# Kernel tuning notes

Measured on AMD Instinct MI355X. Metric: run time of the kernel, lower is better.

## Reference

```python
import jax, jax.numpy as jnp
import numpy as np

N = 100000       # nodes
E = 1600000      # edges
V = 50000        # vocab
H = 256          # embedding dim (hsize)
A = 64           # per-head out dim (asize)
NH = 3           # num_heads
G = 64           # graphs in batch


def setup_inputs() -> dict:
    key = jax.random.key(0)
    ks = jax.random.split(key, 12)
    h0 = jax.random.randint(ks[0], (N,), 0, V)
    src = jax.random.randint(ks[1], (E,), 0, N)
    dst = jax.random.randint(ks[2], (E,), 0, N)
    graph_ids = jnp.sort(jax.random.randint(ks[3], (N,), 0, G))
    s = 0.05
    emb = jax.random.normal(ks[4], (V, H), jnp.float32) * s
    W_fc = jax.random.normal(ks[5], (H, NH * A), jnp.float32) * s   # GATConv fc
    attn_l = jax.random.normal(ks[6], (NH, A), jnp.float32) * s
    attn_r = jax.random.normal(ks[7], (NH, A), jnp.float32) * s
    bias_gat = jax.random.normal(ks[8], (NH, A), jnp.float32) * s
    W1 = jax.random.normal(ks[9], (A, 128), jnp.float32) * s
    b1 = jnp.zeros((128,), jnp.float32)
    W2 = jax.random.normal(ks[10], (128, 16), jnp.float32) * s
    b2 = jnp.zeros((16,), jnp.float32)
    return dict(h0=h0, src=src, dst=dst, graph_ids=graph_ids, emb=emb,
                W_fc=W_fc, attn_l=attn_l, attn_r=attn_r, bias_gat=bias_gat,
                W1=W1, b1=b1, W2=W2, b2=b2)


def reference(h0, src, dst, graph_ids, emb, W_fc, attn_l, attn_r, bias_gat,
              W1, b1, W2, b2):
    # embedding lookup
    h1 = emb[h0]                                            # [N, H]
    # GATConv: linear projection per head
    feat = (h1 @ W_fc).reshape(N, NH, A)                    # [N, NH, A]
    el = jnp.einsum('nha,ha->nh', feat, attn_l)             # [N, NH]
    er = jnp.einsum('nha,ha->nh', feat, attn_r)             # [N, NH]
    e = jax.nn.leaky_relu(el[src] + er[dst], 0.2)           # [E, NH]
    # segment softmax over incoming edges of each dst node
    m = jax.ops.segment_max(e, dst, num_segments=N)         # [N, NH]
    e_exp = jnp.exp(e - m[dst])                             # [E, NH]
    denom = jax.ops.segment_sum(e_exp, dst, num_segments=N) # [N, NH]
    alpha = e_exp / denom[dst]                              # [E, NH]
    # scatter-aggregate messages
    msg = alpha[:, :, None] * feat[src]                     # [E, NH, A]
    rst = jax.ops.segment_sum(msg, dst, num_segments=N)     # [N, NH, A]
    rst = rst + bias_gat[None]                              # GATConv bias
    # relu + mean over heads
    h2 = jnp.mean(jax.nn.relu(rst), axis=1)                 # [N, A]
    # MLP predictor: ReLU then Identity
    h3 = jax.nn.relu(h2 @ W1 + b1) @ W2 + b2                # [N, 16]
    # dgl.mean_nodes: per-graph mean readout
    sums = jax.ops.segment_sum(h3, graph_ids, num_segments=G)            # [G, 16]
    counts = jax.ops.segment_sum(jnp.ones((N,), h3.dtype), graph_ids, num_segments=G)
    return sums / jnp.maximum(counts, 1.0)[:, None]         # [G, 16]
```

## Files before the change

kernel.cpp:

```cpp
#include <hip/hip_runtime.h>
#include <hip/hip_bf16.h>

#define NNODES 100000
#define NEDGES 1600000
#define VOCAB 50000
#define HDIM 256
#define ADIM 64
#define NHEADS 3
#define FDIM 192
#define NGRAPH 64
#define NPART 64

#define CONV_ELEMS (HDIM * FDIM + 128 * 64 + 16 * 128)
#define CONV_BLOCKS ((CONV_ELEMS + 255) / 256)
#define ELVR_BLOCKS ((VOCAB + 3) / 4)
#define HIST_BLOCKS ((NEDGES + 255) / 256)
#define PROJ_BLOCKS ((VOCAB + 63) / 64)

typedef __attribute__((ext_vector_type(8))) short bf16x8;
typedef __attribute__((ext_vector_type(4))) float f32x4;

__device__ __forceinline__ float bf2f(unsigned short u) {
  return __uint_as_float((unsigned int)u << 16);
}
__device__ __forceinline__ unsigned short f2bf(float f) {
  unsigned int u = __float_as_uint(f);
  u += 0x7FFFu + ((u >> 16) & 1u);
  return (unsigned short)(u >> 16);
}

__global__ __launch_bounds__(256) void prep_kernel(
    const float* __restrict__ Wfc, const float* __restrict__ al,
    const float* __restrict__ ar, float* __restrict__ wl, float* __restrict__ wr)
{
  int t = blockIdx.x * 256 + threadIdx.x;
  if (t >= 3 * 256) return;
  int h = t >> 8, k = t & 255;
  const float* a_l = &al[h * 64];
  const float* a_r = &ar[h * 64];
  const float* row = &Wfc[(size_t)k * FDIM + h * 64];
  float sl = 0.f, sr = 0.f;
#pragma unroll 16
  for (int c = 0; c < 64; ++c) {
    float w = row[c];
    sl += w * a_l[c];
    sr += w * a_r[c];
  }
  wl[h * 256 + k] = sl;
  wr[h * 256 + k] = sr;
}

__global__ __launch_bounds__(256) void conv_elvr_hist_kernel(
    const float* __restrict__ Wfc, const float* __restrict__ W1,
    const float* __restrict__ W2, unsigned short* __restrict__ Wt,
    unsigned short* __restrict__ W1t, unsigned short* __restrict__ W2t,
    const float* __restrict__ emb, const float* __restrict__ wl,
    const float* __restrict__ wr, float4* __restrict__ elv4,
    float4* __restrict__ erv4,
    const int* __restrict__ dst, int* __restrict__ cnt,
    unsigned short* __restrict__ rank16)
{
  if (blockIdx.x < CONV_BLOCKS) {
    int i = blockIdx.x * 256 + threadIdx.x;
    if (i < HDIM * FDIM) {
      int c = i / HDIM, k = i % HDIM;
      Wt[i] = f2bf(Wfc[(size_t)k * FDIM + c]);
    } else if (i < HDIM * FDIM + 128 * 64) {
      int j = i - HDIM * FDIM;
      int c = j / 64, k = j % 64;
      W1t[j] = f2bf(W1[(size_t)k * 128 + c]);
    } else if (i < CONV_ELEMS) {
      int j = i - HDIM * FDIM - 128 * 64;
      int c = j / 128, k = j % 128;
      W2t[j] = f2bf(W2[(size_t)k * 16 + c]);
    }
    return;
  }
  if (blockIdx.x < CONV_BLOCKS + ELVR_BLOCKS) {
    int v = (blockIdx.x - CONV_BLOCKS) * 4 + (threadIdx.x >> 6);
    int lane = threadIdx.x & 63;
    if (v >= VOCAB) return;
    const float* er_ = &emb[(size_t)v * HDIM];
    float e0 = er_[lane], e1 = er_[64 + lane], e2 = er_[128 + lane], e3 = er_[192 + lane];
    float sl[3], sr[3];
#pragma unroll
    for (int h = 0; h < 3; ++h) {
      const float* wlh = &wl[h * 256];
      const float* wrh = &wr[h * 256];
      sl[h] = e0 * wlh[lane] + e1 * wlh[64 + lane] + e2 * wlh[128 + lane] + e3 * wlh[192 + lane];
      sr[h] = e0 * wrh[lane] + e1 * wrh[64 + lane] + e2 * wrh[128 + lane] + e3 * wrh[192 + lane];
    }
#pragma unroll
    for (int s = 32; s > 0; s >>= 1) {
#pragma unroll
      for (int h = 0; h < 3; ++h) {
        sl[h] += __shfl_xor(sl[h], s, 64);
        sr[h] += __shfl_xor(sr[h], s, 64);
      }
    }
    if (lane == 0) {
      elv4[v] = make_float4(sl[0], sl[1], sl[2], 0.f);
      erv4[v] = make_float4(sr[0], sr[1], sr[2], 0.f);
    }
    return;
  }
  int e = (blockIdx.x - CONV_BLOCKS - ELVR_BLOCKS) * 256 + threadIdx.x;
  if (e < NEDGES) rank16[e] = (unsigned short)atomicAdd(&cnt[dst[e]], 1);
}

__global__ __launch_bounds__(256) void scan_sum_kernel(
    const int* __restrict__ cnt, int* __restrict__ bsum, int n)
{
  __shared__ int red[256];
  int t = threadIdx.x;
  int base = blockIdx.x * 1024 + t * 4;
  int s = 0;
#pragma unroll
  for (int j = 0; j < 4; ++j) if (base + j < n) s += cnt[base + j];
  red[t] = s;
  __syncthreads();
  for (int o = 128; o > 0; o >>= 1) {
    if (t < o) red[t] += red[t + o];
    __syncthreads();
  }
  if (t == 0) bsum[blockIdx.x] = red[0];
}

__global__ void scan_bsum_kernel(int* bsum, int nb)
{
  if (threadIdx.x == 0 && blockIdx.x == 0) {
    int acc = 0;
    for (int i = 0; i < nb; ++i) { int v = bsum[i]; bsum[i] = acc; acc += v; }
  }
}

__global__ __launch_bounds__(256) void scan_write_kernel(
    const int* __restrict__ cnt, const int* __restrict__ bsum,
    int* __restrict__ offs, int n, int total)
{
  __shared__ int sd[256];
  int t = threadIdx.x;
  int base = blockIdx.x * 1024 + t * 4;
  int c[4];
  int ts = 0;
#pragma unroll
  for (int j = 0; j < 4; ++j) { c[j] = (base + j < n) ? cnt[base + j] : 0; ts += c[j]; }
  sd[t] = ts;
  __syncthreads();
  for (int o = 1; o < 256; o <<= 1) {
    int v = (t >= o) ? sd[t - o] : 0;
    __syncthreads();
    sd[t] += v;
    __syncthreads();
  }
  int run = sd[t] - ts + bsum[blockIdx.x];
#pragma unroll
  for (int j = 0; j < 4; ++j) {
    if (base + j < n) offs[base + j] = run;
    run += c[j];
  }
  if (blockIdx.x == 0 && t == 0) offs[n] = total;
}

__global__ __launch_bounds__(256) void proj_scatter_kernel(
    const float* __restrict__ emb,
    const unsigned short* __restrict__ Wt,
    unsigned short* __restrict__ proj_bf,
    const int* __restrict__ src, const int* __restrict__ dst,
    const int* __restrict__ h0, const unsigned short* __restrict__ rank16,
    const int* __restrict__ offs,
    const float4* __restrict__ elv4, const float4* __restrict__ erv4,
    uint2* __restrict__ wrec)
{
  if (blockIdx.x >= PROJ_BLOCKS) {
    int e = (blockIdx.x - PROJ_BLOCKS) * 256 + threadIdx.x;
    if (e < NEDGES) {
      int s = src[e], d = dst[e];
      unsigned vs = (unsigned)h0[s];
      float4 el = elv4[vs];
      float4 er = erv4[(unsigned)h0[d]];
      float e0 = el.x + er.x, e1 = el.y + er.y, e2 = el.z + er.z;
      e0 = e0 > 0.f ? e0 : 0.2f * e0;
      e1 = e1 > 0.f ? e1 : 0.2f * e1;
      e2 = e2 > 0.f ? e2 : 0.2f * e2;
      unsigned short u0 = f2bf(__expf(e0));
      unsigned short u1 = f2bf(__expf(e1));
      unsigned short u2 = f2bf(__expf(e2));
      int p = offs[d] + (int)rank16[e];
      wrec[p] = make_uint2(vs | ((unsigned)u0 << 16),
                           (unsigned)u1 | ((unsigned)u2 << 16));
    }
    return;
  }
  const int wave = threadIdx.x >> 6;
  const int lane = threadIdx.x & 63;
  const int row0 = blockIdx.x * 64 + wave * 16;
  const int cb = lane & 15;
  const int q  = lane >> 4;
  int arow = row0 + cb;
  if (arow >= VOCAB) arow = VOCAB - 1;
  const int kgrp = q * 8;

  f32x4 acc[12];
#pragma unroll
  for (int c = 0; c < 12; ++c) acc[c] = (f32x4){0.f, 0.f, 0.f, 0.f};

  const float* arow_p = &emb[(size_t)arow * HDIM + kgrp];
  const unsigned short* bcol_p = &Wt[(size_t)cb * HDIM + kgrp];

#pragma unroll
  for (int ks = 0; ks < 8; ++ks) {
    float4 f0 = *reinterpret_cast<const float4*>(arow_p + ks * 32);
    float4 f1 = *reinterpret_cast<const float4*>(arow_p + ks * 32 + 4);
    bf16x8 a;
    a[0] = (short)f2bf(f0.x); a[1] = (short)f2bf(f0.y);
    a[2] = (short)f2bf(f0.z); a[3] = (short)f2bf(f0.w);
    a[4] = (short)f2bf(f1.x); a[5] = (short)f2bf(f1.y);
    a[6] = (short)f2bf(f1.z); a[7] = (short)f2bf(f1.w);
#pragma unroll
    for (int c = 0; c < 12; ++c) {
      bf16x8 b = *reinterpret_cast<const bf16x8*>(bcol_p + (size_t)c * 16 * HDIM + ks * 32);
      acc[c] = __builtin_amdgcn_mfma_f32_16x16x32_bf16(a, b, acc[c], 0, 0, 0);
    }
  }

  const int rb = row0 + 4 * q;
#pragma unroll
  for (int i = 0; i < 4; ++i) {
    int r = rb + i;
    if (r < VOCAB) {
#pragma unroll
      for (int c = 0; c < 12; ++c)
        proj_bf[(size_t)r * FDIM + c * 16 + cb] = f2bf(acc[c][i]);
    }
  }
}

__global__ __launch_bounds__(256) void aggregate_kernel(
    const uint2* __restrict__ wrec, const int* __restrict__ offs,
    const unsigned short* __restrict__ proj_bf, const float* __restrict__ bias_gat,
    unsigned short* __restrict__ h2bf, int N)
{
  int lane = threadIdx.x & 63;
  int n = blockIdx.x * 4 + (threadIdx.x >> 6);
  if (n >= N) return;
  int lo = offs[n], hi = offs[n + 1];
  float a0 = 0.f, a1 = 0.f, a2 = 0.f, d0 = 0.f, d1 = 0.f, d2 = 0.f;

  int i = lo;
  for (; i + 4 <= hi; i += 4) {
    uint2 r[4];
#pragma unroll
    for (int j = 0; j < 4; ++j) r[j] = wrec[i + j];
    const unsigned short* ps[4];
#pragma unroll
    for (int j = 0; j < 4; ++j)
      ps[j] = &proj_bf[(size_t)(r[j].x & 0xFFFFu) * FDIM];
    float g0[4], g1[4], g2[4];
#pragma unroll
    for (int j = 0; j < 4; ++j) {
      g0[j] = bf2f(ps[j][lane]);
      g1[j] = bf2f(ps[j][64 + lane]);
      g2[j] = bf2f(ps[j][128 + lane]);
    }
#pragma unroll
    for (int j = 0; j < 4; ++j) {
      float w0 = bf2f((unsigned short)(r[j].x >> 16));
      float w1 = bf2f((unsigned short)(r[j].y & 0xFFFFu));
      float w2 = bf2f((unsigned short)(r[j].y >> 16));
      a0 += w0 * g0[j]; a1 += w1 * g1[j]; a2 += w2 * g2[j];
      d0 += w0; d1 += w1; d2 += w2;
    }
  }
  for (; i < hi; ++i) {
    uint2 r = wrec[i];
    const unsigned short* ps = &proj_bf[(size_t)(r.x & 0xFFFFu) * FDIM];
    float w0 = bf2f((unsigned short)(r.x >> 16));
    float w1 = bf2f((unsigned short)(r.y & 0xFFFFu));
    float w2 = bf2f((unsigned short)(r.y >> 16));
    a0 += w0 * bf2f(ps[lane]);
    a1 += w1 * bf2f(ps[64 + lane]);
    a2 += w2 * bf2f(ps[128 + lane]);
    d0 += w0; d1 += w1; d2 += w2;
  }

  float i0 = d0 > 0.f ? 1.f / d0 : 0.f;
  float i1 = d1 > 0.f ? 1.f / d1 : 0.f;
  float i2 = d2 > 0.f ? 1.f / d2 : 0.f;
  float r0 = a0 * i0 + bias_gat[lane];
  float r1 = a1 * i1 + bias_gat[64 + lane];
  float r2 = a2 * i2 + bias_gat[128 + lane];
  float h2 = (fmaxf(r0, 0.f) + fmaxf(r1, 0.f) + fmaxf(r2, 0.f)) * (1.f / 3.f);
  h2bf[(size_t)n * 64 + lane] = f2bf(h2);
}

__global__ __launch_bounds__(256) void post_mfma_kernel(
    const unsigned short* __restrict__ h2bf,
    const unsigned short* __restrict__ W1t,
    const float* __restrict__ b1,
    const unsigned short* __restrict__ W2t,
    const float* __restrict__ b2, const int* __restrict__ gid,
    float* __restrict__ sums_priv, float* __restrict__ counts_priv, int N)
{
  __shared__ unsigned short z_lds[64 * 128];
  const int wave = threadIdx.x >> 6;
  const int lane = threadIdx.x & 63;
  const int r = lane & 15;
  const int q = lane >> 4;
  const int kg = q * 8;
  const int rw0 = blockIdx.x * 64 + wave * 16;

  int arow = rw0 + r;
  if (arow >= N) arow = N - 1;

  f32x4 acc1[8];
#pragma unroll
  for (int c = 0; c < 8; ++c) acc1[c] = (f32x4){0.f, 0.f, 0.f, 0.f};

#pragma unroll
  for (int ks = 0; ks < 2; ++ks) {
    bf16x8 a = *reinterpret_cast<const bf16x8*>(&h2bf[(size_t)arow * 64 + kg + ks * 32]);
#pragma unroll
    for (int c = 0; c < 8; ++c) {
      bf16x8 b = *reinterpret_cast<const bf16x8*>(&W1t[(size_t)(c * 16 + r) * 64 + kg + ks * 32]);
      acc1[c] = __builtin_amdgcn_mfma_f32_16x16x32_bf16(a, b, acc1[c], 0, 0, 0);
    }
  }
#pragma unroll
  for (int c = 0; c < 8; ++c) {
    float bb = b1[c * 16 + r];
#pragma unroll
    for (int i = 0; i < 4; ++i) {
      float z = acc1[c][i] + bb;
      z = z > 0.f ? z : 0.f;
      z_lds[(wave * 16 + 4 * q + i) * 128 + c * 16 + r] = f2bf(z);
    }
  }
  __syncthreads();

  f32x4 acc2 = (f32x4){0.f, 0.f, 0.f, 0.f};
#pragma unroll
  for (int ks = 0; ks < 4; ++ks) {
    bf16x8 a = *reinterpret_cast<const bf16x8*>(&z_lds[(wave * 16 + r) * 128 + kg + ks * 32]);
    bf16x8 b = *reinterpret_cast<const bf16x8*>(&W2t[(size_t)r * 128 + kg + ks * 32]);
    acc2 = __builtin_amdgcn_mfma_f32_16x16x32_bf16(a, b, acc2, 0, 0, 0);
  }
  const int part = blockIdx.x & (NPART - 1);
  float bb2 = b2[r];
#pragma unroll
  for (int i = 0; i < 4; ++i) {
    int row = rw0 + 4 * q + i;
    if (row < N) {
      int g = gid[row];
      atomicAdd(&sums_priv[(part * NGRAPH + g) * 16 + r], acc2[i] + bb2);
      if (r == 0) atomicAdd(&counts_priv[part * NGRAPH + g], 1.f);
    }
  }
}

__global__ void finalize_kernel(const float* __restrict__ sums_priv,
                                const float* __restrict__ counts_priv,
                                float* __restrict__ out)
{
  int j = threadIdx.x;
  int g = j >> 4;
  float s = 0.f, c = 0.f;
  for (int p = 0; p < NPART; ++p) {
    s += sums_priv[p * NGRAPH * 16 + j];
    c += counts_priv[p * NGRAPH + g];
  }
  out[j] = s / fmaxf(c, 1.f);
}

extern "C" void kernel_launch(void* const* d_in, const int* in_sizes, int n_in,
                              void* d_out, int out_size, void* d_ws, size_t ws_size,
                              hipStream_t stream)
{
  const int*   h0  = (const int*)  d_in[0];
  const int*   src = (const int*)  d_in[1];
  const int*   dst = (const int*)  d_in[2];
  const int*   gid = (const int*)  d_in[3];
  const float* emb = (const float*)d_in[4];
  const float* Wfc = (const float*)d_in[5];
  const float* al  = (const float*)d_in[6];
  const float* ar  = (const float*)d_in[7];
  const float* bg  = (const float*)d_in[8];
  const float* W1  = (const float*)d_in[9];
  const float* b1  = (const float*)d_in[10];
  const float* W2  = (const float*)d_in[11];
  const float* b2  = (const float*)d_in[12];
  float* out = (float*)d_out;

  char* ws = (char*)d_ws;
  size_t off = 0;
  auto alloc = [&](size_t bytes) -> void* {
    off = (off + 255) & ~(size_t)255;
    void* p = ws + off;
    off += bytes;
    return p;
  };
  const size_t CNT_B  = (size_t)NNODES * 4;
  const size_t CNT_BP = (CNT_B + 255) & ~(size_t)255;
  const size_t SUMS_B = (size_t)NPART * NGRAPH * 16 * 4;
  const size_t ZB     = CNT_BP + SUMS_B + (size_t)NPART * NGRAPH * 4;
  char*  zero_base = (char*)alloc(ZB);
  int*   cnt  = (int*)zero_base;
  float* sums = (float*)(zero_base + CNT_BP);
  float* cnts = (float*)(zero_base + CNT_BP + SUMS_B);

  unsigned short* Wt      = (unsigned short*)alloc((size_t)FDIM * HDIM * 2);
  unsigned short* W1t     = (unsigned short*)alloc((size_t)128 * 64 * 2);
  unsigned short* W2t     = (unsigned short*)alloc((size_t)16 * 128 * 2);
  unsigned short* proj_bf = (unsigned short*)alloc((size_t)VOCAB * FDIM * 2);
  unsigned short* h2bf    = (unsigned short*)alloc((size_t)NNODES * 64 * 2);
  unsigned short* rank16  = (unsigned short*)alloc((size_t)NEDGES * 2);
  uint2*  wrec   = (uint2*) alloc((size_t)NEDGES * 8);
  float4* elv4   = (float4*)alloc((size_t)VOCAB * 16);
  float4* erv4   = (float4*)alloc((size_t)VOCAB * 16);
  float*  wl     = (float*) alloc((size_t)3 * 256 * 4);
  float*  wr     = (float*) alloc((size_t)3 * 256 * 4);
  int*    offs   = (int*)   alloc((size_t)(NNODES + 1) * 4);
  int*    bsum   = (int*)   alloc((size_t)128 * 4);

  hipMemsetAsync(zero_base, 0, ZB, stream);

  const int NB = (NNODES + 1023) / 1024;

  prep_kernel<<<3, 256, 0, stream>>>(Wfc, al, ar, wl, wr);
  conv_elvr_hist_kernel<<<CONV_BLOCKS + ELVR_BLOCKS + HIST_BLOCKS, 256, 0, stream>>>(
      Wfc, W1, W2, Wt, W1t, W2t, emb, wl, wr, elv4, erv4, dst, cnt, rank16);
  scan_sum_kernel<<<NB, 256, 0, stream>>>(cnt, bsum, NNODES);
  scan_bsum_kernel<<<1, 64, 0, stream>>>(bsum, NB);
  scan_write_kernel<<<NB, 256, 0, stream>>>(cnt, bsum, offs, NNODES, NEDGES);
  proj_scatter_kernel<<<PROJ_BLOCKS + HIST_BLOCKS, 256, 0, stream>>>(
      emb, Wt, proj_bf, src, dst, h0, rank16, offs, elv4, erv4, wrec);
  aggregate_kernel<<<(NNODES + 3) / 4, 256, 0, stream>>>(wrec, offs, proj_bf,
                                                         bg, h2bf, NNODES);
  post_mfma_kernel<<<(NNODES + 63) / 64, 256, 0, stream>>>(h2bf, W1t, b1, W2t, b2, gid,
                                                           sums, cnts, NNODES);
  finalize_kernel<<<1, 1024, 0, stream>>>(sums, cnts, out);
}
```

Before: 342.8 us.

## Merge scan passes into single-pass scan and regroup prep/elvr kernels

Replaces the three-kernel prefix scan (block sums, serial bsum scan, write) with one kernel where each block recomputes its base offset by summing all preceding counts. The prep computation moves into the histogram kernel and the el/er vocab projection moves into the scan kernel, cutting the launch count from five to two. This removes launch gaps and the single-thread serial scan. In exchange, every scan block redundantly reads the counts that precede its range.

```diff
diff --git a/kernel.cpp b/kernel.cpp
--- a/kernel.cpp
+++ b/kernel.cpp
@@ -13,9 +13,11 @@
 
 #define CONV_ELEMS (HDIM * FDIM + 128 * 64 + 16 * 128)
 #define CONV_BLOCKS ((CONV_ELEMS + 255) / 256)
+#define HIST_BLOCKS ((NEDGES + 255) / 256)
+#define PREP_BLOCKS 3
 #define ELVR_BLOCKS ((VOCAB + 3) / 4)
-#define HIST_BLOCKS ((NEDGES + 255) / 256)
 #define PROJ_BLOCKS ((VOCAB + 63) / 64)
+#define NB ((NNODES + 1023) / 1024)
 
 typedef __attribute__((ext_vector_type(8))) short bf16x8;
 typedef __attribute__((ext_vector_type(4))) float f32x4;
@@ -29,36 +31,14 @@
   return (unsigned short)(u >> 16);
 }
 
-__global__ __launch_bounds__(256) void prep_kernel(
-    const float* __restrict__ Wfc, const float* __restrict__ al,
-    const float* __restrict__ ar, float* __restrict__ wl, float* __restrict__ wr)
-{
-  int t = blockIdx.x * 256 + threadIdx.x;
-  if (t >= 3 * 256) return;
-  int h = t >> 8, k = t & 255;
-  const float* a_l = &al[h * 64];
-  const float* a_r = &ar[h * 64];
-  const float* row = &Wfc[(size_t)k * FDIM + h * 64];
-  float sl = 0.f, sr = 0.f;
-#pragma unroll 16
-  for (int c = 0; c < 64; ++c) {
-    float w = row[c];
-    sl += w * a_l[c];
-    sr += w * a_r[c];
-  }
-  wl[h * 256 + k] = sl;
-  wr[h * 256 + k] = sr;
-}
-
-__global__ __launch_bounds__(256) void conv_elvr_hist_kernel(
+__global__ __launch_bounds__(256) void conv_hist_prep_kernel(
     const float* __restrict__ Wfc, const float* __restrict__ W1,
     const float* __restrict__ W2, unsigned short* __restrict__ Wt,
     unsigned short* __restrict__ W1t, unsigned short* __restrict__ W2t,
-    const float* __restrict__ emb, const float* __restrict__ wl,
-    const float* __restrict__ wr, float4* __restrict__ elv4,
-    float4* __restrict__ erv4,
     const int* __restrict__ dst, int* __restrict__ cnt,
-    unsigned short* __restrict__ rank16)
+    unsigned short* __restrict__ rank16,
+    const float* __restrict__ al, const float* __restrict__ ar,
+    float* __restrict__ wl, float* __restrict__ wr)
 {
   if (blockIdx.x < CONV_BLOCKS) {
     int i = blockIdx.x * 256 + threadIdx.x;
@@ -76,90 +56,104 @@
     }
     return;
   }
-  if (blockIdx.x < CONV_BLOCKS + ELVR_BLOCKS) {
-    int v = (blockIdx.x - CONV_BLOCKS) * 4 + (threadIdx.x >> 6);
-    int lane = threadIdx.x & 63;
-    if (v >= VOCAB) return;
-    const float* er_ = &emb[(size_t)v * HDIM];
-    float e0 = er_[lane], e1 = er_[64 + lane], e2 = er_[128 + lane], e3 = er_[192 + lane];
-    float sl[3], sr[3];
+  if (blockIdx.x < CONV_BLOCKS + HIST_BLOCKS) {
+    int e = (blockIdx.x - CONV_BLOCKS) * 256 + threadIdx.x;
+    if (e < NEDGES) rank16[e] = (unsigned short)atomicAdd(&cnt[dst[e]], 1);
+    return;
+  }
+  int t = (blockIdx.x - CONV_BLOCKS - HIST_BLOCKS) * 256 + threadIdx.x;
+  if (t >= 3 * 256) return;
+  int h = t >> 8, k = t & 255;
+  const float* a_l = &al[h * 64];
+  const float* a_r = &ar[h * 64];
+  const float* row = &Wfc[(size_t)k * FDIM + h * 64];
+  float sl = 0.f, sr = 0.f;
+#pragma unroll 16
+  for (int c = 0; c < 64; ++c) {
+    float w = row[c];
+    sl += w * a_l[c];
+    sr += w * a_r[c];
+  }
+  wl[h * 256 + k] = sl;
+  wr[h * 256 + k] = sr;
+}
+
+__global__ __launch_bounds__(256) void scan_elvr_kernel(
+    const int* __restrict__ cnt, int* __restrict__ offs,
+    const float* __restrict__ emb, const float* __restrict__ wl,
+    const float* __restrict__ wr, float4* __restrict__ elv4,
+    float4* __restrict__ erv4)
+{
+  if (blockIdx.x < NB) {
+    __shared__ int sd[256];
+    __shared__ int base_sh;
+    const int i = blockIdx.x, t = threadIdx.x;
+    const int pre = i * 1024;
+    int s = 0;
+    for (int j = t * 4; j < pre; j += 1024) {
+      int4 v = *reinterpret_cast<const int4*>(&cnt[j]);
+      s += v.x + v.y + v.z + v.w;
+    }
+    sd[t] = s;
+    __syncthreads();
+    for (int o = 128; o > 0; o >>= 1) {
+      if (t < o) sd[t] += sd[t + o];
+      __syncthreads();
+    }
+    if (t == 0) base_sh = sd[0];
+    __syncthreads();
+    const int base = base_sh;
+    __syncthreads();
+    int bstart = pre + t * 4;
+    int c[4];
+    int ts = 0;
+#pragma unroll
+    for (int j = 0; j < 4; ++j) {
+      c[j] = (bstart + j < NNODES) ? cnt[bstart + j] : 0;
+      ts += c[j];
+    }
+    sd[t] = ts;
+    __syncthreads();
+    for (int o = 1; o < 256; o <<= 1) {
+      int v = (t >= o) ? sd[t - o] : 0;
+      __syncthreads();
+      sd[t] += v;
+      __syncthreads();
+    }
+    int run = sd[t] - ts + base;
+#pragma unroll
+    for (int j = 0; j < 4; ++j) {
+      if (bstart + j < NNODES) offs[bstart + j] = run;
+      run += c[j];
+    }
+    if (i == NB - 1 && t == 255) offs[NNODES] = base + sd[255];
+    return;
+  }
+  int v = (blockIdx.x - NB) * 4 + (threadIdx.x >> 6);
+  int lane = threadIdx.x & 63;
+  if (v >= VOCAB) return;
+  const float* er_ = &emb[(size_t)v * HDIM];
+  float e0 = er_[lane], e1 = er_[64 + lane], e2 = er_[128 + lane], e3 = er_[192 + lane];
+  float sl[3], sr[3];
+#pragma unroll
+  for (int h = 0; h < 3; ++h) {
+    const float* wlh = &wl[h * 256];
+    const float* wrh = &wr[h * 256];
+    sl[h] = e0 * wlh[lane] + e1 * wlh[64 + lane] + e2 * wlh[128 + lane] + e3 * wlh[192 + lane];
+    sr[h] = e0 * wrh[lane] + e1 * wrh[64 + lane] + e2 * wrh[128 + lane] + e3 * wrh[192 + lane];
+  }
+#pragma unroll
+  for (int s = 32; s > 0; s >>= 1) {
 #pragma unroll
     for (int h = 0; h < 3; ++h) {
-      const float* wlh = &wl[h * 256];
-      const float* wrh = &wr[h * 256];
-      sl[h] = e0 * wlh[lane] + e1 * wlh[64 + lane] + e2 * wlh[128 + lane] + e3 * wlh[192 + lane];
-      sr[h] = e0 * wrh[lane] + e1 * wrh[64 + lane] + e2 * wrh[128 + lane] + e3 * wrh[192 + lane];
-    }
-#pragma unroll
-    for (int s = 32; s > 0; s >>= 1) {
-#pragma unroll
-      for (int h = 0; h < 3; ++h) {
-        sl[h] += __shfl_xor(sl[h], s, 64);
-        sr[h] += __shfl_xor(sr[h], s, 64);
-      }
-    }
-    if (lane == 0) {
-      elv4[v] = make_float4(sl[0], sl[1], sl[2], 0.f);
-      erv4[v] = make_float4(sr[0], sr[1], sr[2], 0.f);
-    }
-    return;
-  }
-  int e = (blockIdx.x - CONV_BLOCKS - ELVR_BLOCKS) * 256 + threadIdx.x;
-  if (e < NEDGES) rank16[e] = (unsigned short)atomicAdd(&cnt[dst[e]], 1);
-}
-
-__global__ __launch_bounds__(256) void scan_sum_kernel(
-    const int* __restrict__ cnt, int* __restrict__ bsum, int n)
-{
-  __shared__ int red[256];
-  int t = threadIdx.x;
-  int base = blockIdx.x * 1024 + t * 4;
-  int s = 0;
-#pragma unroll
-  for (int j = 0; j < 4; ++j) if (base + j < n) s += cnt[base + j];
-  red[t] = s;
-  __syncthreads();
-  for (int o = 128; o > 0; o >>= 1) {
-    if (t < o) red[t] += red[t + o];
-    __syncthreads();
-  }
-  if (t == 0) bsum[blockIdx.x] = red[0];
-}
-
-__global__ void scan_bsum_kernel(int* bsum, int nb)
-{
-  if (threadIdx.x == 0 && blockIdx.x == 0) {
-    int acc = 0;
-    for (int i = 0; i < nb; ++i) { int v = bsum[i]; bsum[i] = acc; acc += v; }
-  }
-}
-
-__global__ __launch_bounds__(256) void scan_write_kernel(
-    const int* __restrict__ cnt, const int* __restrict__ bsum,
-    int* __restrict__ offs, int n, int total)
-{
-  __shared__ int sd[256];
-  int t = threadIdx.x;
-  int base = blockIdx.x * 1024 + t * 4;
-  int c[4];
-  int ts = 0;
-#pragma unroll
-  for (int j = 0; j < 4; ++j) { c[j] = (base + j < n) ? cnt[base + j] : 0; ts += c[j]; }
-  sd[t] = ts;
-  __syncthreads();
-  for (int o = 1; o < 256; o <<= 1) {
-    int v = (t >= o) ? sd[t - o] : 0;
-    __syncthreads();
-    sd[t] += v;
-    __syncthreads();
-  }
-  int run = sd[t] - ts + bsum[blockIdx.x];
-#pragma unroll
-  for (int j = 0; j < 4; ++j) {
-    if (base + j < n) offs[base + j] = run;
-    run += c[j];
-  }
-  if (blockIdx.x == 0 && t == 0) offs[n] = total;
+      sl[h] += __shfl_xor(sl[h], s, 64);
+      sr[h] += __shfl_xor(sr[h], s, 64);
+    }
+  }
+  if (lane == 0) {
+    elv4[v] = make_float4(sl[0], sl[1], sl[2], 0.f);
+    erv4[v] = make_float4(sr[0], sr[1], sr[2], 0.f);
+  }
 }
 
 __global__ __launch_bounds__(256) void proj_scatter_kernel(
@@ -420,18 +414,13 @@
   float*  wl     = (float*) alloc((size_t)3 * 256 * 4);
   float*  wr     = (float*) alloc((size_t)3 * 256 * 4);
   int*    offs   = (int*)   alloc((size_t)(NNODES + 1) * 4);
-  int*    bsum   = (int*)   alloc((size_t)128 * 4);
 
   hipMemsetAsync(zero_base, 0, ZB, stream);
 
-  const int NB = (NNODES + 1023) / 1024;
-
-  prep_kernel<<<3, 256, 0, stream>>>(Wfc, al, ar, wl, wr);
-  conv_elvr_hist_kernel<<<CONV_BLOCKS + ELVR_BLOCKS + HIST_BLOCKS, 256, 0, stream>>>(
-      Wfc, W1, W2, Wt, W1t, W2t, emb, wl, wr, elv4, erv4, dst, cnt, rank16);
-  scan_sum_kernel<<<NB, 256, 0, stream>>>(cnt, bsum, NNODES);
-  scan_bsum_kernel<<<1, 64, 0, stream>>>(bsum, NB);
-  scan_write_kernel<<<NB, 256, 0, stream>>>(cnt, bsum, offs, NNODES, NEDGES);
+  conv_hist_prep_kernel<<<CONV_BLOCKS + HIST_BLOCKS + PREP_BLOCKS, 256, 0, stream>>>(
+      Wfc, W1, W2, Wt, W1t, W2t, dst, cnt, rank16, al, ar, wl, wr);
+  scan_elvr_kernel<<<NB + ELVR_BLOCKS, 256, 0, stream>>>(
+      cnt, offs, emb, wl, wr, elv4, erv4);
   proj_scatter_kernel<<<PROJ_BLOCKS + HIST_BLOCKS, 256, 0, stream>>>(
       emb, Wt, proj_bf, src, dst, h0, rank16, offs, elv4, erv4, wrec);
   aggregate_kernel<<<(NNODES + 3) / 4, 256, 0, stream>>>(wrec, offs, proj_bf,
```

Result: faster. 327.8 us (-4.4%).
